# Kernel tuning notes

Hardware: AMD Instinct MI355X
Metric: run time of the kernel (lower is better)

Reference implementation:

```python
import jax, jax.numpy as jnp
import numpy as np

B, H, S = 2, 16, 2048
CTX = 1024
VD = 288          # valence_dim
FFN = 512         # ffn_dim
EPSILON = 0.066
LN_EPS = 1e-5


def layer_norm(x, w, b):
    mu = jnp.mean(x, axis=-1, keepdims=True)
    var = jnp.var(x, axis=-1, keepdims=True)
    return (x - mu) * jax.lax.rsqrt(var + LN_EPS) * w + b


def setup_inputs() -> dict:
    key = jax.random.key(0)
    ks = jax.random.split(key, 12)

    def lin(k, fan_in, fan_out):
        # torch nn.Linear default init: U(-1/sqrt(fan_in), 1/sqrt(fan_in)); stored as [in, out]
        bound = 1.0 / np.sqrt(fan_in)
        k1, k2 = jax.random.split(k)
        W = jax.random.uniform(k1, (fan_in, fan_out), jnp.float32, -bound, bound)
        b = jax.random.uniform(k2, (fan_out,), jnp.float32, -bound, bound)
        return W, b

    attention_scores = jax.random.normal(ks[0], (B, H, S, S), jnp.float32)
    input_ids = jax.random.randint(ks[1], (B, S), 0, CTX)

    # xavier_uniform for embedding weight [CTX, VD]
    xb = np.sqrt(6.0 / (CTX + VD))
    emb_W = jax.random.uniform(ks[2], (CTX, VD), jnp.float32, -xb, xb)

    pW1, pb1 = lin(ks[3], VD, 2 * VD)
    pW2, pb2 = lin(ks[4], 2 * VD, H)
    fW1, fb1 = lin(ks[5], H + 1, FFN)
    fW2, fb2 = lin(ks[6], FFN, FFN // 2)
    fW3, fb3 = lin(ks[7], FFN // 2, 1)

    return {
        "attention_scores": attention_scores,
        "input_ids": input_ids,
        "emb_W": emb_W,
        "ln_v_w": jnp.ones((VD,), jnp.float32),
        "ln_v_b": jnp.zeros((VD,), jnp.float32),
        "pW1": pW1, "pb1": pb1, "pW2": pW2, "pb2": pb2,
        "ln_c_w": jnp.ones((H + 1,), jnp.float32),
        "ln_c_b": jnp.zeros((H + 1,), jnp.float32),
        "fW1": fW1, "fb1": fb1, "fW2": fW2, "fb2": fb2, "fW3": fW3, "fb3": fb3,
    }


def reference(attention_scores, input_ids, emb_W, ln_v_w, ln_v_b,
              pW1, pb1, pW2, pb2, ln_c_w, ln_c_b,
              fW1, fb1, fW2, fb2, fW3, fb3):
    # token_occurrence buffer starts at zero: new_occ = 0.87*0 + clamp(counts, 1)
    counts = jnp.bincount(input_ids.reshape(-1), length=CTX).astype(jnp.float32)
    counts = jnp.maximum(counts, 1.0)
    occ = jnp.log1p(counts[input_ids])                        # [B, S]

    v = layer_norm(emb_W[input_ids], ln_v_w, ln_v_b)           # [B, S, VD]
    h = jax.nn.gelu(v @ pW1 + pb1, approximate=False)          # [B, S, 2*VD]
    valence_scores = jnp.tanh(h @ pW2 + pb2)                   # [B, S, H]

    comb = jnp.concatenate([occ[..., None], valence_scores], axis=-1)  # [B, S, H+1]
    comb = layer_norm(comb, ln_c_w, ln_c_b)

    h2 = jax.nn.gelu(comb @ fW1 + fb1, approximate=False)      # [B, S, FFN]
    h3 = jax.nn.gelu(h2 @ fW2 + fb2, approximate=False)        # [B, S, FFN//2]
    mod = jnp.tanh(h3 @ fW3 + fb3)                             # [B, S, 1]

    retrieval_weights = 1.0 + EPSILON * mod[:, None, :, :]     # [B, 1, S, 1]
    return attention_scores * retrieval_weights
```

## Files before the change

kernel.cpp:

```cpp
#include <hip/hip_runtime.h>
#include <math.h>

#define B_ 2
#define H_ 16
#define S_ 2048
#define CTX_ 1024
#define VD_ 288
#define VD2_ 576
#define FFN_ 512
#define FFNH_ 256
#define NH1_ 17
#define EPSILON_ 0.066f
#define LN_EPS_ 1e-5f
#define TPB_ 16
#define NBLK_ (B_ * S_ / TPB_)

typedef float vfloat4 __attribute__((ext_vector_type(4)));

__device__ __forceinline__ float gelu_exact(float x) {
    return 0.5f * x * (1.0f + erff(x * 0.70710678118654752440f));
}
__device__ __forceinline__ vfloat4 gelu4(vfloat4 v) {
    vfloat4 o;
    o.x = gelu_exact(v.x); o.y = gelu_exact(v.y);
    o.z = gelu_exact(v.z); o.w = gelu_exact(v.w);
    return o;
}

__global__ __launch_bounds__(1024) void count_kernel(
    const int* __restrict__ ids, int* __restrict__ counts)
{
    __shared__ int hist[CTX_];
    const int t = threadIdx.x;
    hist[t] = 0;
    __syncthreads();
    #pragma unroll
    for (int r = 0; r < (B_ * S_) / 1024; ++r)
        atomicAdd(&hist[ids[t + 1024 * r]], 1);
    __syncthreads();
    counts[t] = hist[t];
}

__global__ __launch_bounds__(512) void token_mlp_kernel(
    const int* __restrict__ ids, const int* __restrict__ counts,
    const float* __restrict__ embW,
    const float* __restrict__ lnvw, const float* __restrict__ lnvb,
    const float* __restrict__ pW1, const float* __restrict__ pb1,
    const float* __restrict__ pW2, const float* __restrict__ pb2,
    const float* __restrict__ lncw, const float* __restrict__ lncb,
    const float* __restrict__ fW1, const float* __restrict__ fb1,
    const float* __restrict__ fW2, const float* __restrict__ fb2,
    const float* __restrict__ fW3, const float* __restrict__ fb3,
    float* __restrict__ wout)
{
    __shared__ __align__(16) float va[VD_][TPB_];
    __shared__ __align__(16) float ha[VD2_][TPB_];
    __shared__ __align__(16) float comb17[NH1_][TPB_];
    __shared__ __align__(16) float h2a[FFN_][TPB_];
    __shared__ __align__(16) float h3a[FFNH_][TPB_];

    const int tid  = threadIdx.x;
    const int tok0 = blockIdx.x * TPB_;
    const int wid  = tid >> 6;
    const int cthr = tid & 63;
    const int t0   = (wid & 3) * 2 + (wid >> 2) * 8;
    const int quad = wid & 3;
    const int ch   = wid >> 2;
    const int tq   = quad * 4;

    {
        const int tt = tid >> 5;
        const int l  = tid & 31;
        const int id = ids[tok0 + tt];
        float x[9];
        float s = 0.f, sq = 0.f;
        #pragma unroll
        for (int r = 0; r < 9; ++r) {
            float xv = embW[id * VD_ + l + 32 * r];
            x[r] = xv; s += xv; sq += xv * xv;
        }
        #pragma unroll
        for (int m = 16; m >= 1; m >>= 1) {
            s  += __shfl_xor(s,  m, 64);
            sq += __shfl_xor(sq, m, 64);
        }
        float mu   = s * (1.f / VD_);
        float var  = sq * (1.f / VD_) - mu * mu;
        float rstd = rsqrtf(var + LN_EPS_);
        #pragma unroll
        for (int r = 0; r < 9; ++r) {
            int i = l + 32 * r;
            va[i][tt] = (x[r] - mu) * rstd * lnvw[i] + lnvb[i];
        }
    }
    __syncthreads();

    {
        vfloat4 a0 = 0, a1 = 0, a2 = 0, a3 = 0, a4 = 0;
        const int cb = (VD2_ / 2) * ch;
        const bool extra = (cthr < 32);
        for (int k = 0; k < VD_; k += 4) {
            float w0[4], w1[4], w2[4], w3[4], w4[4];
            #pragma unroll
            for (int u = 0; u < 4; ++u) {
                const float* wr = &pW1[(k + u) * VD2_ + cb + cthr];
                w0[u] = wr[0];   w1[u] = wr[64];
                w2[u] = wr[128]; w3[u] = wr[192];
                if (extra) w4[u] = wr[256];
            }
            vfloat4 v[4];
            #pragma unroll
            for (int u = 0; u < 4; ++u) v[u] = *(const vfloat4*)&va[k + u][tq];
            #pragma unroll
            for (int u = 0; u < 4; ++u) {
                a0 += w0[u] * v[u]; a1 += w1[u] * v[u];
                a2 += w2[u] * v[u]; a3 += w3[u] * v[u];
                if (extra) a4 += w4[u] * v[u];
            }
        }
        int col = cb + cthr;
        *(vfloat4*)&ha[col      ][tq] = gelu4(a0 + pb1[col]);
        *(vfloat4*)&ha[col +  64][tq] = gelu4(a1 + pb1[col + 64]);
        *(vfloat4*)&ha[col + 128][tq] = gelu4(a2 + pb1[col + 128]);
        *(vfloat4*)&ha[col + 192][tq] = gelu4(a3 + pb1[col + 192]);
        if (extra)
            *(vfloat4*)&ha[col + 256][tq] = gelu4(a4 + pb1[col + 256]);
    }
    __syncthreads();

    {
        const int col = cthr & 15;
        const int ks  = cthr >> 4;
        float2 acc = make_float2(0.f, 0.f);
        for (int k = ks * 144; k < ks * 144 + 144; k += 8) {
            float w[8]; float2 v[8];
            #pragma unroll
            for (int u = 0; u < 8; ++u) w[u] = pW2[(k + u) * H_ + col];
            #pragma unroll
            for (int u = 0; u < 8; ++u) v[u] = *(const float2*)&ha[k + u][t0];
            #pragma unroll
            for (int u = 0; u < 8; ++u) {
                acc.x += w[u] * v[u].x; acc.y += w[u] * v[u].y;
            }
        }
        acc.x += __shfl_xor(acc.x, 16, 64); acc.y += __shfl_xor(acc.y, 16, 64);
        acc.x += __shfl_xor(acc.x, 32, 64); acc.y += __shfl_xor(acc.y, 32, 64);
        if (cthr < 16) {
            float b = pb2[col];
            float2 o = make_float2(tanhf(acc.x + b), tanhf(acc.y + b));
            *(float2*)&comb17[1 + col][t0] = o;
        }
        if (cthr == 16) {
            #pragma unroll
            for (int j = 0; j < 2; ++j) {
                int t = t0 + j;
                int id = ids[tok0 + t];
                float c = (float)counts[id];
                if (c < 1.f) c = 1.f;
                comb17[0][t] = log1pf(c);
            }
        }
    }
    __syncthreads();

    if (tid < TPB_) {
        float vals[NH1_];
        float s = 0.f;
        #pragma unroll
        for (int i = 0; i < NH1_; ++i) { vals[i] = comb17[i][tid]; s += vals[i]; }
        float mu = s / NH1_;
        float vq = 0.f;
        #pragma unroll
        for (int i = 0; i < NH1_; ++i) { float d = vals[i] - mu; vq += d * d; }
        float r = rsqrtf(vq / NH1_ + LN_EPS_);
        #pragma unroll
        for (int i = 0; i < NH1_; ++i)
            comb17[i][tid] = (vals[i] - mu) * r * lncw[i] + lncb[i];
    }
    __syncthreads();

    {
        vfloat4 a0 = 0, a1 = 0, a2 = 0, a3 = 0;
        const int cb = (FFN_ / 2) * ch;
        #pragma unroll
        for (int k = 0; k < NH1_; ++k) {
            vfloat4 v = *(const vfloat4*)&comb17[k][tq];
            const float* wrow = &fW1[k * FFN_ + cb + cthr];
            a0 += wrow[0] * v; a1 += wrow[64] * v;
            a2 += wrow[128] * v; a3 += wrow[192] * v;
        }
        int col = cb + cthr;
        *(vfloat4*)&h2a[col      ][tq] = gelu4(a0 + fb1[col]);
        *(vfloat4*)&h2a[col +  64][tq] = gelu4(a1 + fb1[col + 64]);
        *(vfloat4*)&h2a[col + 128][tq] = gelu4(a2 + fb1[col + 128]);
        *(vfloat4*)&h2a[col + 192][tq] = gelu4(a3 + fb1[col + 192]);
    }
    __syncthreads();

    {
        vfloat4 a0 = 0, a1 = 0;
        const int cb = (FFNH_ / 2) * ch;
        for (int k = 0; k < FFN_; k += 8) {
            float w0[8], w1[8]; vfloat4 v[8];
            #pragma unroll
            for (int u = 0; u < 8; ++u) {
                const float* wr = &fW2[(k + u) * FFNH_ + cb + cthr];
                w0[u] = wr[0]; w1[u] = wr[64];
            }
            #pragma unroll
            for (int u = 0; u < 8; ++u) v[u] = *(const vfloat4*)&h2a[k + u][tq];
            #pragma unroll
            for (int u = 0; u < 8; ++u) {
                a0 += w0[u] * v[u];
                a1 += w1[u] * v[u];
            }
        }
        int col = cb + cthr;
        *(vfloat4*)&h3a[col     ][tq] = gelu4(a0 + fb2[col]);
        *(vfloat4*)&h3a[col + 64][tq] = gelu4(a1 + fb2[col + 64]);
    }
    __syncthreads();

    {
        const int tt = tid >> 5;
        const int l  = tid & 31;
        float acc = 0.f;
        #pragma unroll
        for (int r = 0; r < FFNH_ / 32; ++r) {
            int k = l + 32 * r;
            acc += h3a[k][tt] * fW3[k];
        }
        #pragma unroll
        for (int m = 16; m >= 1; m >>= 1) acc += __shfl_xor(acc, m, 64);
        if (l == 0) {
            float mod = tanhf(acc + fb3[0]);
            wout[tok0 + tt] = 1.0f + EPSILON_ * mod;
        }
    }
}

__global__ __launch_bounds__(256) void scale_kernel(
    const vfloat4* __restrict__ in, const float* __restrict__ w,
    vfloat4* __restrict__ out, long total4)
{
    long i = (long)blockIdx.x * blockDim.x + threadIdx.x;
    const long stride = (long)gridDim.x * blockDim.x;
    for (; i < total4; i += stride) {
        long row = i >> 9;
        int b = (int)(row >> 15);
        int s = (int)(row & (S_ - 1));
        float ww = w[b * S_ + s];
        vfloat4 x = __builtin_nontemporal_load(&in[i]);
        x *= ww;
        __builtin_nontemporal_store(x, &out[i]);
    }
}

extern "C" void kernel_launch(void* const* d_in, const int* in_sizes, int n_in,
                              void* d_out, int out_size, void* d_ws, size_t ws_size,
                              hipStream_t stream) {
    const float* scores = (const float*)d_in[0];
    const int*   ids    = (const int*)  d_in[1];
    const float* embW   = (const float*)d_in[2];
    const float* lnvw   = (const float*)d_in[3];
    const float* lnvb   = (const float*)d_in[4];
    const float* pW1    = (const float*)d_in[5];
    const float* pb1    = (const float*)d_in[6];
    const float* pW2    = (const float*)d_in[7];
    const float* pb2    = (const float*)d_in[8];
    const float* lncw   = (const float*)d_in[9];
    const float* lncb   = (const float*)d_in[10];
    const float* fW1    = (const float*)d_in[11];
    const float* fb1    = (const float*)d_in[12];
    const float* fW2    = (const float*)d_in[13];
    const float* fb2    = (const float*)d_in[14];
    const float* fW3    = (const float*)d_in[15];
    const float* fb3    = (const float*)d_in[16];

    int*   counts = (int*)d_ws;
    float* wout   = (float*)((char*)d_ws + CTX_ * sizeof(int));

    count_kernel<<<1, 1024, 0, stream>>>(ids, counts);
    token_mlp_kernel<<<NBLK_, 512, 0, stream>>>(
        ids, counts, embW, lnvw, lnvb, pW1, pb1, pW2, pb2,
        lncw, lncb, fW1, fb1, fW2, fb2, fW3, fb3, wout);

    long total4 = (long)B_ * H_ * S_ * S_ / 4;
    scale_kernel<<<2048, 256, 0, stream>>>(
        (const vfloat4*)scores, wout, (vfloat4*)d_out, total4);
}
```

Before: 284.5 us.

## Halve tokens per block and alias shared buffers to raise MLP occupancy

The token MLP kernel now processes 8 tokens per block instead of 16. Each wave handles 2 tokens with float2 accumulators instead of 4 with vfloat4. Shared-memory buffers are aliased (va with h3a, ha with h2a) to cut LDS footprint, and launch bounds request 4 blocks per CU. The aim is more resident blocks and more blocks overall, trading away some reuse of each weight load across tokens, so weight traffic per token roughly doubles.

```diff
diff --git a/kernel.cpp b/kernel.cpp
--- a/kernel.cpp
+++ b/kernel.cpp
@@ -12,19 +12,13 @@
 #define NH1_ 17
 #define EPSILON_ 0.066f
 #define LN_EPS_ 1e-5f
-#define TPB_ 16
+#define TPB_ 8
 #define NBLK_ (B_ * S_ / TPB_)
 
 typedef float vfloat4 __attribute__((ext_vector_type(4)));
 
 __device__ __forceinline__ float gelu_exact(float x) {
     return 0.5f * x * (1.0f + erff(x * 0.70710678118654752440f));
-}
-__device__ __forceinline__ vfloat4 gelu4(vfloat4 v) {
-    vfloat4 o;
-    o.x = gelu_exact(v.x); o.y = gelu_exact(v.y);
-    o.z = gelu_exact(v.z); o.w = gelu_exact(v.w);
-    return o;
 }
 
 __global__ __launch_bounds__(1024) void count_kernel(
@@ -41,7 +35,7 @@
     counts[t] = hist[t];
 }
 
-__global__ __launch_bounds__(512) void token_mlp_kernel(
+__global__ __launch_bounds__(512, 4) void token_mlp_kernel(
     const int* __restrict__ ids, const int* __restrict__ counts,
     const float* __restrict__ embW,
     const float* __restrict__ lnvw, const float* __restrict__ lnvb,
@@ -53,34 +47,39 @@
     const float* __restrict__ fW3, const float* __restrict__ fb3,
     float* __restrict__ wout)
 {
-    __shared__ __align__(16) float va[VD_][TPB_];
-    __shared__ __align__(16) float ha[VD2_][TPB_];
+    __shared__ __align__(16) char smem[9216 + 18432];
     __shared__ __align__(16) float comb17[NH1_][TPB_];
-    __shared__ __align__(16) float h2a[FFN_][TPB_];
-    __shared__ __align__(16) float h3a[FFNH_][TPB_];
+    float (*va )[TPB_] = (float(*)[TPB_])(smem);
+    float (*h3a)[TPB_] = (float(*)[TPB_])(smem);
+    float (*ha )[TPB_] = (float(*)[TPB_])(smem + 9216);
+    float (*h2a)[TPB_] = (float(*)[TPB_])(smem + 9216);
 
     const int tid  = threadIdx.x;
     const int tok0 = blockIdx.x * TPB_;
     const int wid  = tid >> 6;
     const int cthr = tid & 63;
-    const int t0   = (wid & 3) * 2 + (wid >> 2) * 8;
-    const int quad = wid & 3;
+    const int pair = wid & 3;
     const int ch   = wid >> 2;
-    const int tq   = quad * 4;
-
-    {
-        const int tt = tid >> 5;
-        const int l  = tid & 31;
-        const int id = ids[tok0 + tt];
-        float x[9];
+    const int t0   = pair * 2;
+
+    {
+        const int w  = wid;
+        const int l  = cthr;
+        const int id = ids[tok0 + w];
+        float x[5];
         float s = 0.f, sq = 0.f;
         #pragma unroll
-        for (int r = 0; r < 9; ++r) {
-            float xv = embW[id * VD_ + l + 32 * r];
+        for (int r = 0; r < 4; ++r) {
+            float xv = embW[id * VD_ + l + 64 * r];
             x[r] = xv; s += xv; sq += xv * xv;
         }
-        #pragma unroll
-        for (int m = 16; m >= 1; m >>= 1) {
+        x[4] = 0.f;
+        if (l < 32) {
+            float xv = embW[id * VD_ + 256 + l];
+            x[4] = xv; s += xv; sq += xv * xv;
+        }
+        #pragma unroll
+        for (int m = 32; m >= 1; m >>= 1) {
             s  += __shfl_xor(s,  m, 64);
             sq += __shfl_xor(sq, m, 64);
         }
@@ -88,15 +87,19 @@
         float var  = sq * (1.f / VD_) - mu * mu;
         float rstd = rsqrtf(var + LN_EPS_);
         #pragma unroll
-        for (int r = 0; r < 9; ++r) {
-            int i = l + 32 * r;
-            va[i][tt] = (x[r] - mu) * rstd * lnvw[i] + lnvb[i];
-        }
-    }
-    __syncthreads();
-
-    {
-        vfloat4 a0 = 0, a1 = 0, a2 = 0, a3 = 0, a4 = 0;
+        for (int r = 0; r < 4; ++r) {
+            int i = l + 64 * r;
+            va[i][w] = (x[r] - mu) * rstd * lnvw[i] + lnvb[i];
+        }
+        if (l < 32) {
+            int i = 256 + l;
+            va[i][w] = (x[4] - mu) * rstd * lnvw[i] + lnvb[i];
+        }
+    }
+    __syncthreads();
+
+    {
+        float2 a0 = {0,0}, a1 = {0,0}, a2 = {0,0}, a3 = {0,0}, a4 = {0,0};
         const int cb = (VD2_ / 2) * ch;
         const bool extra = (cthr < 32);
         for (int k = 0; k < VD_; k += 4) {
@@ -108,27 +111,36 @@
                 w2[u] = wr[128]; w3[u] = wr[192];
                 if (extra) w4[u] = wr[256];
             }
-            vfloat4 v[4];
-            #pragma unroll
-            for (int u = 0; u < 4; ++u) v[u] = *(const vfloat4*)&va[k + u][tq];
+            float2 v[4];
+            #pragma unroll
+            for (int u = 0; u < 4; ++u) v[u] = *(const float2*)&va[k + u][t0];
             #pragma unroll
             for (int u = 0; u < 4; ++u) {
-                a0 += w0[u] * v[u]; a1 += w1[u] * v[u];
-                a2 += w2[u] * v[u]; a3 += w3[u] * v[u];
-                if (extra) a4 += w4[u] * v[u];
+                a0.x += w0[u] * v[u].x; a0.y += w0[u] * v[u].y;
+                a1.x += w1[u] * v[u].x; a1.y += w1[u] * v[u].y;
+                a2.x += w2[u] * v[u].x; a2.y += w2[u] * v[u].y;
+                a3.x += w3[u] * v[u].x; a3.y += w3[u] * v[u].y;
+                if (extra) { a4.x += w4[u] * v[u].x; a4.y += w4[u] * v[u].y; }
             }
         }
         int col = cb + cthr;
-        *(vfloat4*)&ha[col      ][tq] = gelu4(a0 + pb1[col]);
-        *(vfloat4*)&ha[col +  64][tq] = gelu4(a1 + pb1[col + 64]);
-        *(vfloat4*)&ha[col + 128][tq] = gelu4(a2 + pb1[col + 128]);
-        *(vfloat4*)&ha[col + 192][tq] = gelu4(a3 + pb1[col + 192]);
-        if (extra)
-            *(vfloat4*)&ha[col + 256][tq] = gelu4(a4 + pb1[col + 256]);
-    }
-    __syncthreads();
-
-    {
+        float2 o;
+        o.x = gelu_exact(a0.x + pb1[col]);       o.y = gelu_exact(a0.y + pb1[col]);
+        *(float2*)&ha[col][t0] = o;
+        o.x = gelu_exact(a1.x + pb1[col + 64]);  o.y = gelu_exact(a1.y + pb1[col + 64]);
+        *(float2*)&ha[col + 64][t0] = o;
+        o.x = gelu_exact(a2.x + pb1[col + 128]); o.y = gelu_exact(a2.y + pb1[col + 128]);
+        *(float2*)&ha[col + 128][t0] = o;
+        o.x = gelu_exact(a3.x + pb1[col + 192]); o.y = gelu_exact(a3.y + pb1[col + 192]);
+        *(float2*)&ha[col + 192][t0] = o;
+        if (extra) {
+            o.x = gelu_exact(a4.x + pb1[col + 256]); o.y = gelu_exact(a4.y + pb1[col + 256]);
+            *(float2*)&ha[col + 256][t0] = o;
+        }
+    }
+    __syncthreads();
+
+    if (ch == 0) {
         const int col = cthr & 15;
         const int ks  = cthr >> 4;
         float2 acc = make_float2(0.f, 0.f);
@@ -180,58 +192,69 @@
     __syncthreads();
 
     {
-        vfloat4 a0 = 0, a1 = 0, a2 = 0, a3 = 0;
+        float2 a0 = {0,0}, a1 = {0,0}, a2 = {0,0}, a3 = {0,0};
         const int cb = (FFN_ / 2) * ch;
         #pragma unroll
         for (int k = 0; k < NH1_; ++k) {
-            vfloat4 v = *(const vfloat4*)&comb17[k][tq];
-            const float* wrow = &fW1[k * FFN_ + cb + cthr];
-            a0 += wrow[0] * v; a1 += wrow[64] * v;
-            a2 += wrow[128] * v; a3 += wrow[192] * v;
+            float2 v = *(const float2*)&comb17[k][t0];
+            const float* wr = &fW1[k * FFN_ + cb + cthr];
+            float w0 = wr[0], w1 = wr[64], w2 = wr[128], w3 = wr[192];
+            a0.x += w0 * v.x; a0.y += w0 * v.y;
+            a1.x += w1 * v.x; a1.y += w1 * v.y;
+            a2.x += w2 * v.x; a2.y += w2 * v.y;
+            a3.x += w3 * v.x; a3.y += w3 * v.y;
         }
         int col = cb + cthr;
-        *(vfloat4*)&h2a[col      ][tq] = gelu4(a0 + fb1[col]);
-        *(vfloat4*)&h2a[col +  64][tq] = gelu4(a1 + fb1[col + 64]);
-        *(vfloat4*)&h2a[col + 128][tq] = gelu4(a2 + fb1[col + 128]);
-        *(vfloat4*)&h2a[col + 192][tq] = gelu4(a3 + fb1[col + 192]);
-    }
-    __syncthreads();
-
-    {
-        vfloat4 a0 = 0, a1 = 0;
+        float2 o;
+        o.x = gelu_exact(a0.x + fb1[col]);       o.y = gelu_exact(a0.y + fb1[col]);
+        *(float2*)&h2a[col][t0] = o;
+        o.x = gelu_exact(a1.x + fb1[col + 64]);  o.y = gelu_exact(a1.y + fb1[col + 64]);
+        *(float2*)&h2a[col + 64][t0] = o;
+        o.x = gelu_exact(a2.x + fb1[col + 128]); o.y = gelu_exact(a2.y + fb1[col + 128]);
+        *(float2*)&h2a[col + 128][t0] = o;
+        o.x = gelu_exact(a3.x + fb1[col + 192]); o.y = gelu_exact(a3.y + fb1[col + 192]);
+        *(float2*)&h2a[col + 192][t0] = o;
+    }
+    __syncthreads();
+
+    {
+        float2 a0 = {0,0}, a1 = {0,0};
         const int cb = (FFNH_ / 2) * ch;
         for (int k = 0; k < FFN_; k += 8) {
-            float w0[8], w1[8]; vfloat4 v[8];
+            float w0[8], w1[8]; float2 v[8];
             #pragma unroll
             for (int u = 0; u < 8; ++u) {
                 const float* wr = &fW2[(k + u) * FFNH_ + cb + cthr];
                 w0[u] = wr[0]; w1[u] = wr[64];
             }
             #pragma unroll
-            for (int u = 0; u < 8; ++u) v[u] = *(const vfloat4*)&h2a[k + u][tq];
+            for (int u = 0; u < 8; ++u) v[u] = *(const float2*)&h2a[k + u][t0];
             #pragma unroll
             for (int u = 0; u < 8; ++u) {
-                a0 += w0[u] * v[u];
-                a1 += w1[u] * v[u];
+                a0.x += w0[u] * v[u].x; a0.y += w0[u] * v[u].y;
+                a1.x += w1[u] * v[u].x; a1.y += w1[u] * v[u].y;
             }
         }
         int col = cb + cthr;
-        *(vfloat4*)&h3a[col     ][tq] = gelu4(a0 + fb2[col]);
-        *(vfloat4*)&h3a[col + 64][tq] = gelu4(a1 + fb2[col + 64]);
-    }
-    __syncthreads();
-
-    {
-        const int tt = tid >> 5;
-        const int l  = tid & 31;
+        float2 o;
+        o.x = gelu_exact(a0.x + fb2[col]);      o.y = gelu_exact(a0.y + fb2[col]);
+        *(float2*)&h3a[col][t0] = o;
+        o.x = gelu_exact(a1.x + fb2[col + 64]); o.y = gelu_exact(a1.y + fb2[col + 64]);
+        *(float2*)&h3a[col + 64][t0] = o;
+    }
+    __syncthreads();
+
+    {
+        const int tt = wid;
+        const int l  = cthr;
         float acc = 0.f;
         #pragma unroll
-        for (int r = 0; r < FFNH_ / 32; ++r) {
-            int k = l + 32 * r;
+        for (int r = 0; r < FFNH_ / 64; ++r) {
+            int k = l + 64 * r;
             acc += h3a[k][tt] * fW3[k];
         }
         #pragma unroll
-        for (int m = 16; m >= 1; m >>= 1) acc += __shfl_xor(acc, m, 64);
+        for (int m = 32; m >= 1; m >>= 1) acc += __shfl_xor(acc, m, 64);
         if (l == 0) {
             float mod = tanhf(acc + fb3[0]);
             wout[tok0 + tt] = 1.0f + EPSILON_ * mod;
```

Measured after the change: 300.0 us. 1.05x slower.

## Halve tokens per block in token MLP and remap warps to column quarters

Applied to the files above, without the earlier changes.

The token MLP kernel now processes 8 tokens per block instead of 16, doubling the grid, and its 8 wavefronts are remapped so each covers a quarter of the output columns for 4 tokens instead of half the columns. LayerNorm and the final reduction now use full 64-lane waves per token, and launch bounds request 4 blocks per CU. The aim is more blocks and better occupancy for the small token MLP, at the cost of loading each weight matrix twice as often across the grid. The large elementwise scale kernel, which probably dominates the time, is unchanged.

```diff
diff --git a/kernel.cpp b/kernel.cpp
--- a/kernel.cpp
+++ b/kernel.cpp
@@ -12,7 +12,7 @@
 #define NH1_ 17
 #define EPSILON_ 0.066f
 #define LN_EPS_ 1e-5f
-#define TPB_ 16
+#define TPB_ 8
 #define NBLK_ (B_ * S_ / TPB_)
 
 typedef float vfloat4 __attribute__((ext_vector_type(4)));
@@ -41,7 +41,7 @@
     counts[t] = hist[t];
 }
 
-__global__ __launch_bounds__(512) void token_mlp_kernel(
+__global__ __launch_bounds__(512, 4) void token_mlp_kernel(
     const int* __restrict__ ids, const int* __restrict__ counts,
     const float* __restrict__ embW,
     const float* __restrict__ lnvw, const float* __restrict__ lnvb,
@@ -63,24 +63,28 @@
     const int tok0 = blockIdx.x * TPB_;
     const int wid  = tid >> 6;
     const int cthr = tid & 63;
-    const int t0   = (wid & 3) * 2 + (wid >> 2) * 8;
-    const int quad = wid & 3;
-    const int ch   = wid >> 2;
+    const int quad = wid & 1;
+    const int cq   = wid >> 1;
     const int tq   = quad * 4;
 
     {
-        const int tt = tid >> 5;
-        const int l  = tid & 31;
-        const int id = ids[tok0 + tt];
-        float x[9];
+        const int w  = wid;
+        const int l  = cthr;
+        const int id = ids[tok0 + w];
+        float x[5];
         float s = 0.f, sq = 0.f;
         #pragma unroll
-        for (int r = 0; r < 9; ++r) {
-            float xv = embW[id * VD_ + l + 32 * r];
+        for (int r = 0; r < 4; ++r) {
+            float xv = embW[id * VD_ + l + 64 * r];
             x[r] = xv; s += xv; sq += xv * xv;
         }
-        #pragma unroll
-        for (int m = 16; m >= 1; m >>= 1) {
+        x[4] = 0.f;
+        if (l < 32) {
+            float xv = embW[id * VD_ + 256 + l];
+            x[4] = xv; s += xv; sq += xv * xv;
+        }
+        #pragma unroll
+        for (int m = 32; m >= 1; m >>= 1) {
             s  += __shfl_xor(s,  m, 64);
             sq += __shfl_xor(sq, m, 64);
         }
@@ -88,47 +92,49 @@
         float var  = sq * (1.f / VD_) - mu * mu;
         float rstd = rsqrtf(var + LN_EPS_);
         #pragma unroll
-        for (int r = 0; r < 9; ++r) {
-            int i = l + 32 * r;
-            va[i][tt] = (x[r] - mu) * rstd * lnvw[i] + lnvb[i];
-        }
-    }
-    __syncthreads();
-
-    {
-        vfloat4 a0 = 0, a1 = 0, a2 = 0, a3 = 0, a4 = 0;
-        const int cb = (VD2_ / 2) * ch;
-        const bool extra = (cthr < 32);
+        for (int r = 0; r < 4; ++r) {
+            int i = l + 64 * r;
+            va[i][w] = (x[r] - mu) * rstd * lnvw[i] + lnvb[i];
+        }
+        if (l < 32) {
+            int i = 256 + l;
+            va[i][w] = (x[4] - mu) * rstd * lnvw[i] + lnvb[i];
+        }
+    }
+    __syncthreads();
+
+    {
+        vfloat4 a0 = 0, a1 = 0, a2 = 0;
+        const int cb = 144 * cq;
+        const bool extra = (cthr < 16);
         for (int k = 0; k < VD_; k += 4) {
-            float w0[4], w1[4], w2[4], w3[4], w4[4];
+            float w0[4], w1[4], w2[4];
             #pragma unroll
             for (int u = 0; u < 4; ++u) {
                 const float* wr = &pW1[(k + u) * VD2_ + cb + cthr];
-                w0[u] = wr[0];   w1[u] = wr[64];
-                w2[u] = wr[128]; w3[u] = wr[192];
-                if (extra) w4[u] = wr[256];
+                w0[u] = wr[0]; w1[u] = wr[64];
+                if (extra) w2[u] = wr[128];
             }
             vfloat4 v[4];
             #pragma unroll
             for (int u = 0; u < 4; ++u) v[u] = *(const vfloat4*)&va[k + u][tq];
             #pragma unroll
             for (int u = 0; u < 4; ++u) {
-                a0 += w0[u] * v[u]; a1 += w1[u] * v[u];
-                a2 += w2[u] * v[u]; a3 += w3[u] * v[u];
-                if (extra) a4 += w4[u] * v[u];
+                a0 += w0[u] * v[u];
+                a1 += w1[u] * v[u];
+                if (extra) a2 += w2[u] * v[u];
             }
         }
         int col = cb + cthr;
-        *(vfloat4*)&ha[col      ][tq] = gelu4(a0 + pb1[col]);
-        *(vfloat4*)&ha[col +  64][tq] = gelu4(a1 + pb1[col + 64]);
-        *(vfloat4*)&ha[col + 128][tq] = gelu4(a2 + pb1[col + 128]);
-        *(vfloat4*)&ha[col + 192][tq] = gelu4(a3 + pb1[col + 192]);
+        *(vfloat4*)&ha[col     ][tq] = gelu4(a0 + pb1[col]);
+        *(vfloat4*)&ha[col + 64][tq] = gelu4(a1 + pb1[col + 64]);
         if (extra)
-            *(vfloat4*)&ha[col + 256][tq] = gelu4(a4 + pb1[col + 256]);
-    }
-    __syncthreads();
-
-    {
+            *(vfloat4*)&ha[col + 128][tq] = gelu4(a2 + pb1[col + 128]);
+    }
+    __syncthreads();
+
+    if (wid < 4) {
+        const int t0  = wid * 2;
         const int col = cthr & 15;
         const int ks  = cthr >> 4;
         float2 acc = make_float2(0.f, 0.f);
@@ -180,58 +186,50 @@
     __syncthreads();
 
     {
-        vfloat4 a0 = 0, a1 = 0, a2 = 0, a3 = 0;
-        const int cb = (FFN_ / 2) * ch;
+        vfloat4 a0 = 0, a1 = 0;
+        const int cb = 128 * cq;
         #pragma unroll
         for (int k = 0; k < NH1_; ++k) {
             vfloat4 v = *(const vfloat4*)&comb17[k][tq];
-            const float* wrow = &fW1[k * FFN_ + cb + cthr];
-            a0 += wrow[0] * v; a1 += wrow[64] * v;
-            a2 += wrow[128] * v; a3 += wrow[192] * v;
+            const float* wr = &fW1[k * FFN_ + cb + cthr];
+            a0 += wr[0] * v;
+            a1 += wr[64] * v;
         }
         int col = cb + cthr;
-        *(vfloat4*)&h2a[col      ][tq] = gelu4(a0 + fb1[col]);
-        *(vfloat4*)&h2a[col +  64][tq] = gelu4(a1 + fb1[col + 64]);
-        *(vfloat4*)&h2a[col + 128][tq] = gelu4(a2 + fb1[col + 128]);
-        *(vfloat4*)&h2a[col + 192][tq] = gelu4(a3 + fb1[col + 192]);
-    }
-    __syncthreads();
-
-    {
-        vfloat4 a0 = 0, a1 = 0;
-        const int cb = (FFNH_ / 2) * ch;
+        *(vfloat4*)&h2a[col     ][tq] = gelu4(a0 + fb1[col]);
+        *(vfloat4*)&h2a[col + 64][tq] = gelu4(a1 + fb1[col + 64]);
+    }
+    __syncthreads();
+
+    {
+        vfloat4 a0 = 0;
+        const int cb = 64 * cq;
         for (int k = 0; k < FFN_; k += 8) {
-            float w0[8], w1[8]; vfloat4 v[8];
-            #pragma unroll
-            for (int u = 0; u < 8; ++u) {
-                const float* wr = &fW2[(k + u) * FFNH_ + cb + cthr];
-                w0[u] = wr[0]; w1[u] = wr[64];
-            }
+            float w0[8]; vfloat4 v[8];
+            #pragma unroll
+            for (int u = 0; u < 8; ++u)
+                w0[u] = fW2[(k + u) * FFNH_ + cb + cthr];
             #pragma unroll
             for (int u = 0; u < 8; ++u) v[u] = *(const vfloat4*)&h2a[k + u][tq];
             #pragma unroll
-            for (int u = 0; u < 8; ++u) {
-                a0 += w0[u] * v[u];
-                a1 += w1[u] * v[u];
-            }
+            for (int u = 0; u < 8; ++u) a0 += w0[u] * v[u];
         }
         int col = cb + cthr;
-        *(vfloat4*)&h3a[col     ][tq] = gelu4(a0 + fb2[col]);
-        *(vfloat4*)&h3a[col + 64][tq] = gelu4(a1 + fb2[col + 64]);
-    }
-    __syncthreads();
-
-    {
-        const int tt = tid >> 5;
-        const int l  = tid & 31;
+        *(vfloat4*)&h3a[col][tq] = gelu4(a0 + fb2[col]);
+    }
+    __syncthreads();
+
+    {
+        const int tt = wid;
+        const int l  = cthr;
         float acc = 0.f;
         #pragma unroll
-        for (int r = 0; r < FFNH_ / 32; ++r) {
-            int k = l + 32 * r;
+        for (int r = 0; r < FFNH_ / 64; ++r) {
+            int k = l + 64 * r;
             acc += h3a[k][tt] * fW3[k];
         }
         #pragma unroll
-        for (int m = 16; m >= 1; m >>= 1) acc += __shfl_xor(acc, m, 64);
+        for (int m = 32; m >= 1; m >>= 1) acc += __shfl_xor(acc, m, 64);
         if (l == 0) {
             float mod = tanhf(acc + fb3[0]);
             wout[tok0 + tt] = 1.0f + EPSILON_ * mod;
```

After: 273.9 us. 1.04x faster.
